# Kernel optimization log

Hardware: AMD Instinct MI355X
Metric: run time of the kernel (lower is better)

Reference implementation:

```python
import jax, jax.numpy as jnp
import numpy as np

H = 16  # heads


def setup_inputs() -> dict:
    key = jax.random.key(0)
    ks = jax.random.split(key, 10)
    B, S, M = 4, 2048, 1024
    scale = 1.0 / np.sqrt(M)
    return {
        "x": jax.random.normal(ks[0], (B, S, M), dtype=jnp.float32),
        "mask": jax.random.uniform(ks[1], (B, 1, S, S), dtype=jnp.float32),
        "Wq": jax.random.normal(ks[2], (M, M), dtype=jnp.float32) * scale,
        "bq": jax.random.normal(ks[3], (M,), dtype=jnp.float32) * scale,
        "Wk": jax.random.normal(ks[4], (M, M), dtype=jnp.float32) * scale,
        "bk": jax.random.normal(ks[5], (M,), dtype=jnp.float32) * scale,
        "Wv": jax.random.normal(ks[6], (M, M), dtype=jnp.float32) * scale,
        "bv": jax.random.normal(ks[7], (M,), dtype=jnp.float32) * scale,
        "Wo": jax.random.normal(ks[8], (M, M), dtype=jnp.float32) * scale,
        "bo": jax.random.normal(ks[9], (M,), dtype=jnp.float32) * scale,
    }


def reference(x, mask, Wq, bq, Wk, bk, Wv, bv, Wo, bo):
    B, S, M = x.shape
    dk = M // H
    # QKV projections (torch Linear: x @ W.T + b), then split heads -> [B,H,S,dk]
    q = (x @ Wq.T + bq).reshape(B, S, H, dk).transpose(0, 2, 1, 3)
    k = (x @ Wk.T + bk).reshape(B, S, H, dk).transpose(0, 2, 1, 3)
    v = (x @ Wv.T + bv).reshape(B, S, H, dk).transpose(0, 2, 1, 3)
    # scores: [B,H,S,S], multiplicative mask (non-standard!) then softmax
    scores = jnp.einsum("bhqd,bhkd->bhqk", q, k) / jnp.sqrt(jnp.float32(dk))
    scores = scores * mask  # mask broadcasts over heads
    attn = jax.nn.softmax(scores, axis=-1)
    # dropout is identity in eval/reference mode
    out = jnp.einsum("bhqk,bhkd->bhqd", attn, v)  # [B,H,S,dk]
    concat = out.transpose(0, 2, 1, 3).reshape(B, S, M)
    return concat @ Wo.T + bo
```

## Files before the change

### kernel.cpp

```cpp
#include <hip/hip_runtime.h>

typedef __attribute__((ext_vector_type(8))) short s16x8;
typedef __attribute__((ext_vector_type(4))) short s16x4;
typedef __attribute__((ext_vector_type(4))) float f32x4;
typedef __attribute__((ext_vector_type(16))) float f32x16;
typedef __attribute__((ext_vector_type(2))) unsigned int u32x2;

#define DEV static __device__ __forceinline__

DEV void gload_lds16(const void* g, void* l) {
  __builtin_amdgcn_global_load_lds(
      (const __attribute__((address_space(1))) void*)g,
      (__attribute__((address_space(3))) void*)l, 16, 0, 0);
}

DEV unsigned short f2bf(float f) {
  unsigned int u = __float_as_uint(f);
  u = (u + 0x7fffu + ((u >> 16) & 1u)) >> 16;
  return (unsigned short)u;
}

DEV float bf2f(unsigned short u) { return __uint_as_float((unsigned)u << 16); }

DEV unsigned pk2(float lo, float hi) {
  unsigned r;
  asm("v_cvt_pk_bf16_f32 %0, %1, %2" : "=v"(r) : "v"(lo), "v"(hi));
  return r;
}

DEV float exp2_fast(float x) {
  float r;
  asm("v_exp_f32 %0, %1" : "=v"(r) : "v"(x));
  return r;
}

DEV void cvt8(const float* __restrict__ in, unsigned short* __restrict__ out, int i) {
  float4 a = *(const float4*)(in + i);
  float4 b = *(const float4*)(in + i + 4);
  union { s16x8 v; unsigned short u[8]; } o;
  o.u[0] = f2bf(a.x); o.u[1] = f2bf(a.y); o.u[2] = f2bf(a.z); o.u[3] = f2bf(a.w);
  o.u[4] = f2bf(b.x); o.u[5] = f2bf(b.y); o.u[6] = f2bf(b.z); o.u[7] = f2bf(b.w);
  *(s16x8*)(out + i) = o.v;
}

__global__ __launch_bounds__(256) void k_cvt_all(
    const float* __restrict__ x, const float* __restrict__ Wq,
    const float* __restrict__ Wk, const float* __restrict__ Wv,
    const float* __restrict__ Wo, unsigned short* __restrict__ xb,
    unsigned short* __restrict__ wcat) {
  const int bid = blockIdx.x;
  if (bid < 4096) {
    cvt8(x, xb, (bid * 256 + threadIdx.x) * 8);
  } else {
    const int id = bid - 4096;
    const int sel = id >> 9;
    const float* in = (sel == 0) ? Wq : (sel == 1) ? Wk : (sel == 2) ? Wv : Wo;
    cvt8(in, wcat + sel * 1048576, ((id & 511) * 256 + threadIdx.x) * 8);
  }
}

__global__ __launch_bounds__(256) void k_gemm_qkv(
    const unsigned short* __restrict__ A, const unsigned short* __restrict__ Bcat,
    const float* __restrict__ bq, const float* __restrict__ bk,
    const float* __restrict__ bv,
    unsigned short* __restrict__ outQK, unsigned short* __restrict__ vtw) {
  constexpr int K = 1024;
  __shared__ unsigned short As[128 * 64];
  __shared__ unsigned short Bs[128 * 64];

  const int lin = blockIdx.x;
  const int logical = (lin & 7) * 192 + (lin >> 3);
  const int nb = logical % 24;
  const int mb = logical / 24;
  const int m0 = mb * 128;
  const int n0 = nb * 128;
  const int z = n0 >> 10;

  const int tid = threadIdx.x;
  const int lane = tid & 63;
  const int l15 = lane & 15, g = lane >> 4;
  const int w = tid >> 6;
  const int wr = w >> 1, wc = w & 1;

  const int sr = tid >> 3;
  const int sc = tid & 7;

  f32x4 acc[4][4] = {};

  for (int kt = 0; kt < K / 64; ++kt) {
#pragma unroll
    for (int i = 0; i < 4; ++i) {
      const int row = i * 32 + sr;
      gload_lds16(A + (size_t)(m0 + row) * K + kt * 64 + ((sc ^ (row & 7)) * 8),
                  (void*)(As + i * 2048 + tid * 8));
      gload_lds16(Bcat + (size_t)(n0 + row) * K + kt * 64 + ((sc ^ (row & 7)) * 8),
                  (void*)(Bs + i * 2048 + tid * 8));
    }
    __syncthreads();
#pragma unroll
    for (int ks = 0; ks < 2; ++ks) {
      s16x8 af[4], bf[4];
#pragma unroll
      for (int i = 0; i < 4; ++i) {
        const int ra = wr * 64 + i * 16 + l15;
        af[i] = *(const s16x8*)(As + ra * 64 + (((ks * 4 + g) ^ (ra & 7)) * 8));
        const int rb = wc * 64 + i * 16 + l15;
        bf[i] = *(const s16x8*)(Bs + rb * 64 + (((ks * 4 + g) ^ (rb & 7)) * 8));
      }
#pragma unroll
      for (int i = 0; i < 4; ++i)
#pragma unroll
        for (int j = 0; j < 4; ++j)
          acc[i][j] = __builtin_amdgcn_mfma_f32_16x16x32_bf16(af[i], bf[j], acc[i][j], 0, 0, 0);
    }
    __syncthreads();
  }

  const float* bias = (z == 0) ? bq : (z == 1) ? bk : bv;
#pragma unroll
  for (int j = 0; j < 4; ++j) {
    const int gcol = n0 + wc * 64 + j * 16 + l15;
    const int col = gcol & 1023;
    const float bvv = bias[col];
    const int h = col >> 6, d = col & 63;
#pragma unroll
    for (int i = 0; i < 4; ++i) {
      const int grow0 = m0 + wr * 64 + i * 16 + g * 4;
      const int bb = grow0 >> 11, s0 = grow0 & 2047;
      if (z < 2) {
        unsigned short* outp = outQK + (size_t)z * 8388608;
#pragma unroll
        for (int r = 0; r < 4; ++r)
          outp[(((size_t)(bb * 16 + h) * 2048 + (s0 + r)) << 6) + d] =
              f2bf(acc[i][j][r] + bvv);
      } else {
        union { s16x4 v; unsigned short u[4]; } pk;
#pragma unroll
        for (int r = 0; r < 4; ++r) pk.u[r] = f2bf(acc[i][j][r] + bvv);
        *(s16x4*)(vtw + (((size_t)(bb * 16 + h)) << 17) + (size_t)d * 2048 + s0) = pk.v;
      }
    }
  }
}

__global__ __launch_bounds__(256) void k_gemm_o(
    const unsigned short* __restrict__ A, const unsigned short* __restrict__ Bw,
    const float* __restrict__ bias, float* __restrict__ outp) {
  constexpr int K = 1024;
  __shared__ unsigned short As[128 * 64];
  __shared__ unsigned short Bs[64 * 64];

  const int lin = blockIdx.x;
  const int logical = (lin & 7) * 128 + (lin >> 3);
  const int nb = logical & 15;
  const int mb = logical >> 4;
  const int m0 = mb * 128, n0 = nb * 64;

  const int tid = threadIdx.x;
  const int lane = tid & 63;
  const int l15 = lane & 15, g = lane >> 4;
  const int w = tid >> 6;
  const int wr = w >> 1, wc = w & 1;

  const int sr = tid >> 3;
  const int sc = tid & 7;

  f32x4 acc[4][2] = {};

  for (int kt = 0; kt < K / 64; ++kt) {
#pragma unroll
    for (int i = 0; i < 4; ++i) {
      const int row = i * 32 + sr;
      gload_lds16(A + (size_t)(m0 + row) * K + kt * 64 + ((sc ^ (row & 7)) * 8),
                  (void*)(As + i * 2048 + tid * 8));
    }
#pragma unroll
    for (int i = 0; i < 2; ++i) {
      const int row = i * 32 + sr;
      gload_lds16(Bw + (size_t)(n0 + row) * K + kt * 64 + ((sc ^ (row & 7)) * 8),
                  (void*)(Bs + i * 2048 + tid * 8));
    }
    __syncthreads();
#pragma unroll
    for (int ks = 0; ks < 2; ++ks) {
      s16x8 af[4], bf[2];
#pragma unroll
      for (int mi = 0; mi < 4; ++mi) {
        const int ra = wr * 64 + mi * 16 + l15;
        af[mi] = *(const s16x8*)(As + ra * 64 + (((ks * 4 + g) ^ (ra & 7)) * 8));
      }
#pragma unroll
      for (int nj = 0; nj < 2; ++nj) {
        const int rb = wc * 32 + nj * 16 + l15;
        bf[nj] = *(const s16x8*)(Bs + rb * 64 + (((ks * 4 + g) ^ (rb & 7)) * 8));
      }
#pragma unroll
      for (int mi = 0; mi < 4; ++mi)
#pragma unroll
        for (int nj = 0; nj < 2; ++nj)
          acc[mi][nj] =
              __builtin_amdgcn_mfma_f32_16x16x32_bf16(af[mi], bf[nj], acc[mi][nj], 0, 0, 0);
    }
    __syncthreads();
  }

#pragma unroll
  for (int nj = 0; nj < 2; ++nj) {
    const int gcol = n0 + wc * 32 + nj * 16 + l15;
    const float bv = bias[gcol];
#pragma unroll
    for (int mi = 0; mi < 4; ++mi)
#pragma unroll
      for (int r = 0; r < 4; ++r) {
        const int grow = m0 + wr * 64 + mi * 16 + g * 4 + r;
        outp[(size_t)grow * 1024 + gcol] = acc[mi][nj][r] + bv;
      }
  }
}

__global__ __launch_bounds__(256) void k_maskR(const float* __restrict__ mask,
                                               unsigned short* __restrict__ mR, int b0) {
  constexpr float SC = 0.125f * 1.44269504f;
  const int tid = threadIdx.x;
  const int ql = tid >> 3, c = tid & 7;
  const int q = blockIdx.x * 32 + ql;
  const int t = blockIdx.y;
  const int bz = blockIdx.z;
  const float* src =
      mask + (size_t)(b0 + bz) * 4194304 + (size_t)q * 2048 + t * 64 + c * 8;
  float4 v0 = *(const float4*)src;
  float4 v1 = *(const float4*)(src + 4);
  union { s16x8 v; unsigned short u[8]; } o;
  o.u[0] = f2bf(v0.x * SC); o.u[1] = f2bf(v0.y * SC);
  o.u[2] = f2bf(v0.z * SC); o.u[3] = f2bf(v0.w * SC);
  o.u[4] = f2bf(v1.x * SC); o.u[5] = f2bf(v1.y * SC);
  o.u[6] = f2bf(v1.z * SC); o.u[7] = f2bf(v1.w * SC);
  *(s16x8*)(mR + (size_t)bz * 4194304 + (size_t)t * 131072 + (size_t)q * 64 + c * 8) = o.v;
}

__global__ __launch_bounds__(256) void k_attn3(
    const unsigned short* __restrict__ q, const unsigned short* __restrict__ k,
    const unsigned short* __restrict__ vt, const unsigned short* __restrict__ mR,
    unsigned short* __restrict__ concat, int b0) {
  __shared__ unsigned short Ks[2][64 * 64];
  __shared__ unsigned short Vs[2][64 * 64];
  __shared__ unsigned short Ms[2][128 * 64];

  const int tid = threadIdx.x;
  const int lane = tid & 63;
  const int w = tid >> 6;
  const int l31 = lane & 31;
  const int hh = lane >> 5;

  const int lin = blockIdx.x + 16 * (blockIdx.y + 16 * blockIdx.z);
  const int q8 = (int)(gridDim.z << 8) >> 3;
  const int logical = (lin & 7) * q8 + (lin >> 3);
  const int h = logical & 15;
  const int qt = (logical >> 4) & 15;
  const int bz = logical >> 8;
  const int b = b0 + bz;

  const size_t bhO = (size_t)(b * 16 + h) * (2048 * 64);
  const unsigned short* kb = k + bhO;
  const unsigned short* vb = vt + bhO;
  const int q0 = qt * 128;
  const int qc = w * 32 + l31;
  const int qg = q0 + qc;

  s16x8 qf[4];
  {
    const unsigned short* qp = q + bhO + (size_t)qg * 64 + hh * 8;
#pragma unroll
    for (int kd = 0; kd < 4; ++kd) qf[kd] = *(const s16x8*)(qp + kd * 16);
  }

  const unsigned short* mtb = mR + (size_t)bz * 4194304;

  float m_r = -3.0e38f, l_r = 0.f;
  f32x16 oacc[2] = {};

  const int sr = tid >> 3;
  const int sc = tid & 7;

#define STAGE(BUF, T_)                                                                \
  {                                                                                   \
    const int kv0s = (T_)*64;                                                         \
    _Pragma("unroll") for (int i = 0; i < 2; ++i) {                                   \
      const int row = i * 32 + sr;                                                    \
      const int sz = (sc ^ (row & 7)) * 8;                                            \
      gload_lds16(kb + (size_t)(kv0s + row) * 64 + sz,                                \
                  (void*)(Ks[BUF] + i * 2048 + tid * 8));                             \
      gload_lds16(vb + (size_t)row * 2048 + kv0s + sz,                                \
                  (void*)(Vs[BUF] + i * 2048 + tid * 8));                             \
    }                                                                                 \
    _Pragma("unroll") for (int j = 0; j < 4; ++j) {                                   \
      const int lc = j * 256 + tid;                                                   \
      const int qrow = lc >> 3, cl = lc & 7;                                          \
      gload_lds16(mtb + (size_t)(T_)*131072 + (size_t)(q0 + qrow) * 64 +              \
                      ((cl ^ (qrow & 7)) * 8),                                        \
                  (void*)(Ms[BUF] + lc * 8));                                         \
    }                                                                                 \
  }

  STAGE(0, 0)
  __syncthreads();

  for (int tt = 0; tt < 16; ++tt) {
#pragma unroll
    for (int half = 0; half < 2; ++half) {
      const int t = tt * 2 + half;
      if (t < 31) STAGE(half ^ 1, t + 1)

      f32x16 sacc[2] = {};
      __builtin_amdgcn_s_setprio(1);
#pragma unroll
      for (int f = 0; f < 2; ++f) {
        const int rk = f * 32 + l31;
        const unsigned short* Kr = Ks[half] + rk * 64;
        const int swb = rk & 7;
#pragma unroll
        for (int kd = 0; kd < 4; ++kd) {
          const s16x8 kf = *(const s16x8*)(Kr + (((kd * 2 + hh) ^ swb) * 8));
          sacc[f] = __builtin_amdgcn_mfma_f32_32x32x16_bf16(kf, qf[kd], sacc[f], 0, 0, 0);
        }
      }
      __builtin_amdgcn_s_setprio(0);

      float p[32];
      float tm = -3.0e38f;
      {
        const unsigned short* Mq = Ms[half] + qc * 64 + hh * 4;
        const int sw = qc & 7;
#pragma unroll
        for (int f = 0; f < 2; ++f)
#pragma unroll
          for (int rq = 0; rq < 4; ++rq) {
            const s16x4 m4 = *(const s16x4*)(Mq + (((rq + 4 * f) ^ sw) * 8));
#pragma unroll
            for (int j = 0; j < 4; ++j) {
              const int r = 4 * rq + j;
              const float sv = sacc[f][r] * bf2f((unsigned short)m4[j]);
              p[f * 16 + r] = sv;
              tm = fmaxf(tm, sv);
            }
          }
      }
      tm = fmaxf(tm, __shfl_xor(tm, 32, 64));
      if (__any(tm > m_r + 11.5f)) {
        const float mn = fmaxf(m_r, tm);
        const float rs = exp2_fast(m_r - mn);
        m_r = mn;
        l_r *= rs;
#pragma unroll
        for (int df = 0; df < 2; ++df)
#pragma unroll
          for (int r = 0; r < 16; ++r) oacc[df][r] *= rs;
      }
      float ps = 0.f;
#pragma unroll
      for (int n = 0; n < 32; ++n) {
        p[n] = exp2_fast(p[n] - m_r);
        ps += p[n];
      }
      ps += __shfl_xor(ps, 32, 64);
      l_r += ps;

#pragma unroll
      for (int ks = 0; ks < 4; ++ks) {
        const int pb = ks * 8;
        const unsigned X0 = pk2(p[pb + 0], p[pb + 1]);
        const unsigned X1 = pk2(p[pb + 2], p[pb + 3]);
        const unsigned Y0 = pk2(p[pb + 4], p[pb + 5]);
        const unsigned Y1 = pk2(p[pb + 6], p[pb + 7]);
        const u32x2 r0 = __builtin_amdgcn_permlane32_swap(X0, Y0, false, false);
        const u32x2 r1 = __builtin_amdgcn_permlane32_swap(X1, Y1, false, false);
        union { s16x8 v; unsigned u[4]; } pf;
        pf.u[0] = r0.x; pf.u[1] = r1.x; pf.u[2] = r0.y; pf.u[3] = r1.y;
        __builtin_amdgcn_s_setprio(1);
#pragma unroll
        for (int df = 0; df < 2; ++df) {
          const int rv = df * 32 + l31;
          const s16x8 vf =
              *(const s16x8*)(Vs[half] + rv * 64 + (((ks * 2 + hh) ^ (rv & 7)) * 8));
          oacc[df] = __builtin_amdgcn_mfma_f32_32x32x16_bf16(vf, pf.v, oacc[df], 0, 0, 0);
        }
        __builtin_amdgcn_s_setprio(0);
      }
      __syncthreads();
    }
  }
#undef STAGE

  const float inv = 1.0f / l_r;
  unsigned short* cb = concat + ((size_t)b * 2048 + qg) * 1024 + h * 64;
#pragma unroll
  for (int df = 0; df < 2; ++df)
#pragma unroll
    for (int r = 0; r < 16; r += 2) {
      const int d = df * 32 + (r & 3) + 8 * (r >> 2) + 4 * hh;
      const unsigned u = (unsigned)f2bf(oacc[df][r] * inv) |
                         ((unsigned)f2bf(oacc[df][r + 1] * inv) << 16);
      *(unsigned*)(cb + d) = u;
    }
}

extern "C" void kernel_launch(void* const* d_in, const int* in_sizes, int n_in,
                              void* d_out, int out_size, void* d_ws, size_t ws_size,
                              hipStream_t stream) {
  const float* x    = (const float*)d_in[0];
  const float* mask = (const float*)d_in[1];
  const float* Wq   = (const float*)d_in[2];
  const float* bq   = (const float*)d_in[3];
  const float* Wk   = (const float*)d_in[4];
  const float* bk   = (const float*)d_in[5];
  const float* Wv   = (const float*)d_in[6];
  const float* bv   = (const float*)d_in[7];
  const float* Wo   = (const float*)d_in[8];
  const float* bo   = (const float*)d_in[9];

  char* ws = (char*)d_ws;
  unsigned short* xb    = (unsigned short*)(ws);
  unsigned short* wcat  = (unsigned short*)(ws + (size_t)16777216);
  unsigned short* wob   = wcat + 3 * 1048576;
  unsigned short* qw    = (unsigned short*)(ws + (size_t)25165824);
  unsigned short* kw    = qw + 8388608;
  unsigned short* vtw   = (unsigned short*)(ws + (size_t)58720256);
  unsigned short* mslab = (unsigned short*)(ws + (size_t)75497472);
  unsigned short* cw    = xb;

  k_cvt_all<<<dim3(6144), dim3(256), 0, stream>>>(x, Wq, Wk, Wv, Wo, xb, wcat);
  k_gemm_qkv<<<dim3(1536), dim3(256), 0, stream>>>(xb, wcat, bq, bk, bv, qw, vtw);
  if (ws_size >= (size_t)75497472 + 33554432) {
    k_maskR<<<dim3(64, 32, 4), dim3(256), 0, stream>>>(mask, mslab, 0);
    k_attn3<<<dim3(16, 16, 4), dim3(256), 0, stream>>>(qw, kw, vtw, mslab, cw, 0);
  } else {
    k_maskR<<<dim3(64, 32, 2), dim3(256), 0, stream>>>(mask, mslab, 0);
    k_attn3<<<dim3(16, 16, 2), dim3(256), 0, stream>>>(qw, kw, vtw, mslab, cw, 0);
    k_maskR<<<dim3(64, 32, 2), dim3(256), 0, stream>>>(mask, mslab, 2);
    k_attn3<<<dim3(16, 16, 2), dim3(256), 0, stream>>>(qw, kw, vtw, mslab, cw, 2);
  }
  k_gemm_o<<<dim3(1024), dim3(256), 0, stream>>>(cw, wob, bo, (float*)d_out);
}
```

Measured before the change: 243.9 us.

## Fuse mask loading into attention kernel and fold softmax scale into Q

Removes the separate mask pre-conversion kernel, which read the fp32 mask and wrote a scaled bf16 copy. The attention kernel now reads the fp32 mask directly from global memory into registers, prefetched before each tile's staging. The 1/sqrt(dk)*log2e scale moves into the Q projection epilogue, and the max reduction becomes a tree. This saves one full pass over the mask plus its bf16 write and re-read, at the cost of twice as many mask bytes read inside attention, held in registers that no longer go through LDS.

```diff
diff --git a/kernel.cpp b/kernel.cpp
--- a/kernel.cpp
+++ b/kernel.cpp
@@ -19,8 +19,6 @@
   u = (u + 0x7fffu + ((u >> 16) & 1u)) >> 16;
   return (unsigned short)u;
 }
-
-DEV float bf2f(unsigned short u) { return __uint_as_float((unsigned)u << 16); }
 
 DEV unsigned pk2(float lo, float hi) {
   unsigned r;
@@ -65,6 +63,7 @@
     const float* __restrict__ bv,
     unsigned short* __restrict__ outQK, unsigned short* __restrict__ vtw) {
   constexpr int K = 1024;
+  constexpr float QSC = 0.125f * 1.44269504f;
   __shared__ unsigned short As[128 * 64];
   __shared__ unsigned short Bs[128 * 64];
 
@@ -117,6 +116,7 @@
   }
 
   const float* bias = (z == 0) ? bq : (z == 1) ? bk : bv;
+  const float osc = (z == 0) ? QSC : 1.0f;
 #pragma unroll
   for (int j = 0; j < 4; ++j) {
     const int gcol = n0 + wc * 64 + j * 16 + l15;
@@ -132,7 +132,7 @@
 #pragma unroll
         for (int r = 0; r < 4; ++r)
           outp[(((size_t)(bb * 16 + h) * 2048 + (s0 + r)) << 6) + d] =
-              f2bf(acc[i][j][r] + bvv);
+              f2bf((acc[i][j][r] + bvv) * osc);
       } else {
         union { s16x4 v; unsigned short u[4]; } pk;
 #pragma unroll
@@ -218,33 +218,12 @@
   }
 }
 
-__global__ __launch_bounds__(256) void k_maskR(const float* __restrict__ mask,
-                                               unsigned short* __restrict__ mR, int b0) {
-  constexpr float SC = 0.125f * 1.44269504f;
-  const int tid = threadIdx.x;
-  const int ql = tid >> 3, c = tid & 7;
-  const int q = blockIdx.x * 32 + ql;
-  const int t = blockIdx.y;
-  const int bz = blockIdx.z;
-  const float* src =
-      mask + (size_t)(b0 + bz) * 4194304 + (size_t)q * 2048 + t * 64 + c * 8;
-  float4 v0 = *(const float4*)src;
-  float4 v1 = *(const float4*)(src + 4);
-  union { s16x8 v; unsigned short u[8]; } o;
-  o.u[0] = f2bf(v0.x * SC); o.u[1] = f2bf(v0.y * SC);
-  o.u[2] = f2bf(v0.z * SC); o.u[3] = f2bf(v0.w * SC);
-  o.u[4] = f2bf(v1.x * SC); o.u[5] = f2bf(v1.y * SC);
-  o.u[6] = f2bf(v1.z * SC); o.u[7] = f2bf(v1.w * SC);
-  *(s16x8*)(mR + (size_t)bz * 4194304 + (size_t)t * 131072 + (size_t)q * 64 + c * 8) = o.v;
-}
-
 __global__ __launch_bounds__(256) void k_attn3(
     const unsigned short* __restrict__ q, const unsigned short* __restrict__ k,
-    const unsigned short* __restrict__ vt, const unsigned short* __restrict__ mR,
-    unsigned short* __restrict__ concat, int b0) {
+    const unsigned short* __restrict__ vt, const float* __restrict__ mask,
+    unsigned short* __restrict__ concat) {
   __shared__ unsigned short Ks[2][64 * 64];
   __shared__ unsigned short Vs[2][64 * 64];
-  __shared__ unsigned short Ms[2][128 * 64];
 
   const int tid = threadIdx.x;
   const int lane = tid & 63;
@@ -253,12 +232,10 @@
   const int hh = lane >> 5;
 
   const int lin = blockIdx.x + 16 * (blockIdx.y + 16 * blockIdx.z);
-  const int q8 = (int)(gridDim.z << 8) >> 3;
-  const int logical = (lin & 7) * q8 + (lin >> 3);
+  const int logical = (lin & 7) * 128 + (lin >> 3);
   const int h = logical & 15;
   const int qt = (logical >> 4) & 15;
-  const int bz = logical >> 8;
-  const int b = b0 + bz;
+  const int b = logical >> 8;
 
   const size_t bhO = (size_t)(b * 16 + h) * (2048 * 64);
   const unsigned short* kb = k + bhO;
@@ -274,7 +251,7 @@
     for (int kd = 0; kd < 4; ++kd) qf[kd] = *(const s16x8*)(qp + kd * 16);
   }
 
-  const unsigned short* mtb = mR + (size_t)bz * 4194304;
+  const float* mlane = mask + (size_t)b * 4194304 + (size_t)qg * 2048 + hh * 4;
 
   float m_r = -3.0e38f, l_r = 0.f;
   f32x16 oacc[2] = {};
@@ -293,13 +270,6 @@
       gload_lds16(vb + (size_t)row * 2048 + kv0s + sz,                                \
                   (void*)(Vs[BUF] + i * 2048 + tid * 8));                             \
     }                                                                                 \
-    _Pragma("unroll") for (int j = 0; j < 4; ++j) {                                   \
-      const int lc = j * 256 + tid;                                                   \
-      const int qrow = lc >> 3, cl = lc & 7;                                          \
-      gload_lds16(mtb + (size_t)(T_)*131072 + (size_t)(q0 + qrow) * 64 +              \
-                      ((cl ^ (qrow & 7)) * 8),                                        \
-                  (void*)(Ms[BUF] + lc * 8));                                         \
-    }                                                                                 \
   }
 
   STAGE(0, 0)
@@ -309,6 +279,15 @@
 #pragma unroll
     for (int half = 0; half < 2; ++half) {
       const int t = tt * 2 + half;
+
+      float4 mvf[8];
+#pragma unroll
+      for (int f = 0; f < 2; ++f)
+#pragma unroll
+        for (int rq = 0; rq < 4; ++rq)
+          mvf[f * 4 + rq] = *(const float4*)(mlane + f * 32 + rq * 8);
+      mlane += 64;
+
       if (t < 31) STAGE(half ^ 1, t + 1)
 
       f32x16 sacc[2] = {};
@@ -327,25 +306,26 @@
       __builtin_amdgcn_s_setprio(0);
 
       float p[32];
-      float tm = -3.0e38f;
-      {
-        const unsigned short* Mq = Ms[half] + qc * 64 + hh * 4;
-        const int sw = qc & 7;
-#pragma unroll
-        for (int f = 0; f < 2; ++f)
-#pragma unroll
-          for (int rq = 0; rq < 4; ++rq) {
-            const s16x4 m4 = *(const s16x4*)(Mq + (((rq + 4 * f) ^ sw) * 8));
-#pragma unroll
-            for (int j = 0; j < 4; ++j) {
-              const int r = 4 * rq + j;
-              const float sv = sacc[f][r] * bf2f((unsigned short)m4[j]);
-              p[f * 16 + r] = sv;
-              tm = fmaxf(tm, sv);
-            }
-          }
-      }
+#pragma unroll
+      for (int f = 0; f < 2; ++f)
+#pragma unroll
+        for (int rq = 0; rq < 4; ++rq)
+#pragma unroll
+          for (int j = 0; j < 4; ++j)
+            p[f * 16 + rq * 4 + j] = sacc[f][rq * 4 + j] * mvf[f * 4 + rq][j];
+
+      float a3[11];
+#pragma unroll
+      for (int i = 0; i < 10; ++i)
+        a3[i] = fmaxf(fmaxf(p[3 * i], p[3 * i + 1]), p[3 * i + 2]);
+      a3[10] = fmaxf(p[30], p[31]);
+      const float b0 = fmaxf(fmaxf(a3[0], a3[1]), a3[2]);
+      const float b1 = fmaxf(fmaxf(a3[3], a3[4]), a3[5]);
+      const float b2 = fmaxf(fmaxf(a3[6], a3[7]), a3[8]);
+      const float b3 = fmaxf(a3[9], a3[10]);
+      float tm = fmaxf(fmaxf(fmaxf(b0, b1), b2), b3);
       tm = fmaxf(tm, __shfl_xor(tm, 32, 64));
+
       if (__any(tm > m_r + 11.5f)) {
         const float mn = fmaxf(m_r, tm);
         const float rs = exp2_fast(m_r - mn);
@@ -425,19 +405,10 @@
   unsigned short* qw    = (unsigned short*)(ws + (size_t)25165824);
   unsigned short* kw    = qw + 8388608;
   unsigned short* vtw   = (unsigned short*)(ws + (size_t)58720256);
-  unsigned short* mslab = (unsigned short*)(ws + (size_t)75497472);
   unsigned short* cw    = xb;
 
   k_cvt_all<<<dim3(6144), dim3(256), 0, stream>>>(x, Wq, Wk, Wv, Wo, xb, wcat);
   k_gemm_qkv<<<dim3(1536), dim3(256), 0, stream>>>(xb, wcat, bq, bk, bv, qw, vtw);
-  if (ws_size >= (size_t)75497472 + 33554432) {
-    k_maskR<<<dim3(64, 32, 4), dim3(256), 0, stream>>>(mask, mslab, 0);
-    k_attn3<<<dim3(16, 16, 4), dim3(256), 0, stream>>>(qw, kw, vtw, mslab, cw, 0);
-  } else {
-    k_maskR<<<dim3(64, 32, 2), dim3(256), 0, stream>>>(mask, mslab, 0);
-    k_attn3<<<dim3(16, 16, 2), dim3(256), 0, stream>>>(qw, kw, vtw, mslab, cw, 0);
-    k_maskR<<<dim3(64, 32, 2), dim3(256), 0, stream>>>(mask, mslab, 2);
-    k_attn3<<<dim3(16, 16, 2), dim3(256), 0, stream>>>(qw, kw, vtw, mslab, cw, 2);
-  }
+  k_attn3<<<dim3(16, 16, 4), dim3(256), 0, stream>>>(qw, kw, vtw, mask, cw);
   k_gemm_o<<<dim3(1024), dim3(256), 0, stream>>>(cw, wob, bo, (float*)d_out);
 }
```

Result: slower. 256.8 us (+5.3%).
